# Kernel tuning notes

Hardware: AMD Instinct MI355X
Metric: run time of the kernel (lower is better)

Reference implementation:

```python
import jax, jax.numpy as jnp
import numpy as np

D_IN, D_DICT, K, N = 768, 16384, 32, 8192


def setup_inputs() -> dict:
    key = jax.random.key(0)
    k1, k2, k3, k4, k5 = jax.random.split(key, 5)
    s_in = 1.0 / np.sqrt(D_IN)
    s_dict = 1.0 / np.sqrt(D_DICT)
    return {
        "x": jax.random.normal(k1, (N, D_IN), dtype=jnp.float32),
        # torch Linear: weight [out, in], bias [out]
        "W_enc": jax.random.uniform(k2, (D_DICT, D_IN), jnp.float32, -s_in, s_in),
        "b_enc": jax.random.uniform(k3, (D_DICT,), jnp.float32, -s_in, s_in),
        "W_dec": jax.random.uniform(k4, (D_IN, D_DICT), jnp.float32, -s_dict, s_dict),
        "b_dec": jax.random.uniform(k5, (D_IN,), jnp.float32, -s_dict, s_dict),
    }


def reference(x, W_enc, b_enc, W_dec, b_dec):
    # encode: z = x @ W_enc^T + b_enc  -> [N, d_dict]
    z = jnp.einsum("nd,kd->nk", x, W_enc) + b_enc
    # top-k mask along last dim (scatter 1.0 at top-k indices)
    _, idx = jax.lax.top_k(z, K)                      # idx: [N, K]
    rows = jnp.arange(z.shape[0])[:, None]            # [N, 1]
    mask = jnp.zeros_like(z).at[rows, idx].set(1.0)
    z_sparse = z * mask
    # decode: x_hat = z_sparse @ W_dec^T + b_dec -> [N, d_in]
    x_hat = jnp.einsum("nk,dk->nd", z_sparse, W_dec) + b_dec
    return (x_hat, z_sparse)
```

## Files before the change

### kernel.cpp

```cpp
#include <hip/hip_runtime.h>
#include <stdint.h>

#define D_IN   768
#define D_DICT 16384
#define NROWS  8192
#define TOPK   32
#define CAND_TARGET 40
#define CAND_MAX    80

typedef __attribute__((ext_vector_type(4))) float  f32x4;
typedef __attribute__((ext_vector_type(8))) short  s16x8;
typedef __attribute__((ext_vector_type(4))) unsigned short u16x4;

static __device__ __forceinline__ unsigned short f2bf(float f) {
    unsigned int u = __float_as_uint(f);
    unsigned int r = (u + 0x7FFFu + ((u >> 16) & 1u)) >> 16;
    return (unsigned short)r;
}
static __device__ __forceinline__ unsigned short bfmap(unsigned short u) {
    return (u & 0x8000u) ? (unsigned short)(~u) : (unsigned short)(u | 0x8000u);
}

static __device__ __forceinline__ void gload_lds16(const void* g, void* l) {
    __builtin_amdgcn_global_load_lds(
        (const __attribute__((address_space(1))) unsigned int*)g,
        (__attribute__((address_space(3))) unsigned int*)l, 16, 0, 0);
}

__global__ __launch_bounds__(256) void cast_bf16(const float4* __restrict__ in,
                                                 u16x4* __restrict__ out, int n4) {
    int idx = blockIdx.x * 256 + threadIdx.x;
    if (idx >= n4) return;
    float4 v = in[idx];
    u16x4 o;
    o.x = f2bf(v.x); o.y = f2bf(v.y); o.z = f2bf(v.z); o.w = f2bf(v.w);
    out[idx] = o;
}

__global__ void transpose_wdec(const float* __restrict__ in, float* __restrict__ out) {
    __shared__ float t[32][33];
    int bx = blockIdx.x, by = blockIdx.y;
    int tx = threadIdx.x, ty = threadIdx.y;
#pragma unroll
    for (int i = 0; i < 4; ++i)
        t[ty + i * 8][tx] = in[(size_t)(by * 32 + ty + i * 8) * D_DICT + bx * 32 + tx];
    __syncthreads();
#pragma unroll
    for (int i = 0; i < 4; ++i)
        out[(size_t)(bx * 32 + ty + i * 8) * D_IN + by * 32 + tx] = t[tx][ty + i * 8];
}

__global__ __launch_bounds__(256) void gemm_enc(const unsigned short* __restrict__ Xb,
                                                const unsigned short* __restrict__ Wb,
                                                const float* __restrict__ bEnc,
                                                unsigned short* __restrict__ zhat) {
    __shared__ unsigned short As[128 * 64];
    __shared__ unsigned short Bs[128 * 64];
    const int tid    = threadIdx.x;
    const int waveId = tid >> 6;
    const int lane   = tid & 63;
    const int rowBase = blockIdx.y * 128;
    const int colBase = blockIdx.x * 128;
    const int wm = waveId >> 1, wn = waveId & 1;

    f32x4 acc[4][4] = {};

    const int m0 = wm * 64 + (lane & 15);
    const int n0 = wn * 64 + (lane & 15);
    const int quad = lane >> 4;
    const int xa = m0 & 7;
    const int xb = n0 & 7;

    for (int k0 = 0; k0 < D_IN; k0 += 64) {
#pragma unroll
        for (int i = 0; i < 4; ++i) {
            int slot = i * 256 + tid;
            int r = slot >> 3;
            int cc = ((slot & 7) ^ (r & 7)) * 8;
            const unsigned short* ga = Xb + (size_t)(rowBase + r) * D_IN + k0 + cc;
            const unsigned short* gb = Wb + (size_t)(colBase + r) * D_IN + k0 + cc;
            unsigned short* la = As + (size_t)(i * 256 + waveId * 64) * 8;
            unsigned short* lb = Bs + (size_t)(i * 256 + waveId * 64) * 8;
            gload_lds16(ga, la);
            gload_lds16(gb, lb);
        }
        __syncthreads();
#pragma unroll
        for (int kk = 0; kk < 2; ++kk) {
            const int ch = kk * 4 + quad;
            s16x8 a[4], b[4];
#pragma unroll
            for (int t = 0; t < 4; ++t) {
                a[t] = *(const s16x8*)(As + (m0 + t * 16) * 64 + ((ch ^ xa) << 3));
                b[t] = *(const s16x8*)(Bs + (n0 + t * 16) * 64 + ((ch ^ xb) << 3));
            }
#pragma unroll
            for (int mi = 0; mi < 4; ++mi)
#pragma unroll
                for (int ni = 0; ni < 4; ++ni)
                    acc[mi][ni] = __builtin_amdgcn_mfma_f32_16x16x32_bf16(
                        a[mi], b[ni], acc[mi][ni], 0, 0, 0);
        }
        __syncthreads();
    }

    const int col0 = colBase + wn * 64 + (lane & 15);
    const int rq   = (lane >> 4) * 4;
#pragma unroll
    for (int ni = 0; ni < 4; ++ni) {
        int gc = col0 + ni * 16;
        float bias = bEnc[gc];
#pragma unroll
        for (int mi = 0; mi < 4; ++mi) {
            int gr0 = rowBase + wm * 64 + mi * 16 + rq;
#pragma unroll
            for (int rg = 0; rg < 4; ++rg) {
                float v = acc[mi][ni][rg] + bias;
                zhat[(size_t)(gr0 + rg) * D_DICT + gc] = bfmap(f2bf(v));
            }
        }
    }
}

__global__ __launch_bounds__(256) void sel_dec(const unsigned short* __restrict__ zhat,
                                               const float* __restrict__ x,
                                               const float* __restrict__ wEnc,
                                               const float* __restrict__ bEnc,
                                               const float* __restrict__ wDecT,
                                               const float* __restrict__ bDec,
                                               float* __restrict__ zsp,
                                               float* __restrict__ xhat) {
    const int row = blockIdx.x;
    const int tid = threadIdx.x;
    const int waveId = tid >> 6;

    __shared__ int   histc[4][256];
    __shared__ float xs[D_IN];
    __shared__ int   cidx[CAND_MAX];
    __shared__ float zc[CAND_MAX];
    __shared__ int   selk[TOPK];
    __shared__ float selv[TOPK];
    __shared__ int   sh_bin, sh_cum, sh_bin2;
    __shared__ int   sh_nstrict, sh_ntie, sh_nsel;

    uint4 r[8];
    const uint4* zr4 = (const uint4*)(zhat + (size_t)row * D_DICT);
#pragma unroll
    for (int i = 0; i < 8; ++i) r[i] = zr4[i * 256 + tid];

    {
        float4 z4 = make_float4(0.f, 0.f, 0.f, 0.f);
        float4* zd = (float4*)(zsp + (size_t)row * D_DICT);
#pragma unroll
        for (int i = 0; i < 16; ++i) zd[i * 256 + tid] = z4;
    }

    for (int j = tid; j < D_IN; j += 256) xs[j] = x[(size_t)row * D_IN + j];
    if (tid == 0) { sh_nstrict = 0; sh_ntie = 0; sh_nsel = 0; }

    unsigned int floorU = 0xBF80u;
    int shift1 = 6;
    const int T = CAND_TARGET;

    for (int att = 0; att < 2; ++att) {
        for (int b = tid; b < 1024; b += 256) ((int*)histc)[b] = 0;
        if (tid == 0) sh_bin = -1;
        __syncthreads();
#pragma unroll
        for (int i = 0; i < 8; ++i) {
            unsigned int w[4] = {r[i].x, r[i].y, r[i].z, r[i].w};
#pragma unroll
            for (int q = 0; q < 4; ++q)
#pragma unroll
                for (int h = 0; h < 2; ++h) {
                    unsigned int u = (w[q] >> (16 * h)) & 0xFFFFu;
                    if (u >= floorU) {
                        int bin = (int)((u - floorU) >> shift1);
                        if (bin > 255) bin = 255;
                        atomicAdd(&histc[waveId][bin], 1);
                    }
                }
        }
        __syncthreads();
        if (tid < 256) histc[0][tid] += histc[1][tid] + histc[2][tid] + histc[3][tid];
        __syncthreads();
        if (tid < 64) {
            int l = tid;
            int b0 = 255 - l * 4;
            int s0 = histc[0][b0], s1 = histc[0][b0 - 1],
                s2 = histc[0][b0 - 2], s3 = histc[0][b0 - 3];
            int local = s0 + s1 + s2 + s3;
            int pref = local;
#pragma unroll
            for (int off = 1; off < 64; off <<= 1) {
                int n = __shfl_up(pref, off, 64);
                if (l >= off) pref += n;
            }
            unsigned long long m = __ballot(pref >= T);
            if (m) {
                int first = (int)__ffsll(m) - 1;
                if (l == first) {
                    int cum = pref - local;
                    int b, c;
                    if      (cum + s0 >= T)           { b = b0;     c = cum; }
                    else if (cum + s0 + s1 >= T)      { b = b0 - 1; c = cum + s0; }
                    else if (cum + s0 + s1 + s2 >= T) { b = b0 - 2; c = cum + s0 + s1; }
                    else                              { b = b0 - 3; c = cum + s0 + s1 + s2; }
                    sh_bin = b; sh_cum = c;
                }
            }
        }
        __syncthreads();
        if (sh_bin >= 0) break;
        floorU = 0u; shift1 = 8;
    }
    const int b1 = sh_bin;
    const int cumAbove = sh_cum;
    const int s2 = shift1 - 6;

    for (int b = tid; b < 1024; b += 256) ((int*)histc)[b] = 0;
    __syncthreads();
#pragma unroll
    for (int i = 0; i < 8; ++i) {
        unsigned int w[4] = {r[i].x, r[i].y, r[i].z, r[i].w};
#pragma unroll
        for (int q = 0; q < 4; ++q)
#pragma unroll
            for (int h = 0; h < 2; ++h) {
                unsigned int u = (w[q] >> (16 * h)) & 0xFFFFu;
                if (u >= floorU) {
                    int bin = (int)((u - floorU) >> shift1);
                    if (bin > 255) bin = 255;
                    if (bin == b1) {
                        int bin2 = (int)(((u - floorU) >> s2) & 63u);
                        atomicAdd(&histc[waveId][bin2], 1);
                    }
                }
            }
    }
    __syncthreads();
    if (tid < 64) {
        int l = tid;
        int bb = 63 - l;
        int local = histc[0][bb] + histc[1][bb] + histc[2][bb] + histc[3][bb];
        int pref = local;
#pragma unroll
        for (int off = 1; off < 64; off <<= 1) {
            int n = __shfl_up(pref, off, 64);
            if (l >= off) pref += n;
        }
        unsigned long long m = __ballot(cumAbove + pref >= T);
        int first = (int)__ffsll(m) - 1;
        if (l == first) sh_bin2 = bb;
    }
    __syncthreads();
    const unsigned int tieLo  = floorU + ((unsigned)b1 << shift1) + ((unsigned)sh_bin2 << s2);
    const unsigned int tieTop = tieLo + (1u << s2) - 1u;

#pragma unroll
    for (int i = 0; i < 8; ++i) {
        unsigned int w[4] = {r[i].x, r[i].y, r[i].z, r[i].w};
#pragma unroll
        for (int q = 0; q < 4; ++q)
#pragma unroll
            for (int h = 0; h < 2; ++h) {
                unsigned int u = (w[q] >> (16 * h)) & 0xFFFFu;
                if (u > tieTop) {
                    int p = atomicAdd(&sh_nstrict, 1);
                    cidx[p] = (i * 256 + tid) * 8 + q * 2 + h;
                } else if (u >= tieLo) {
                    int t = atomicAdd(&sh_ntie, 1);
                    if (t < CAND_TARGET) cidx[CAND_MAX - 1 - t] = (i * 256 + tid) * 8 + q * 2 + h;
                }
            }
    }
    __syncthreads();
    const int nstrict = sh_nstrict;
    const int nt = min(sh_ntie, CAND_TARGET);
    int tmpv = 0;
    if (tid < nt) tmpv = cidx[CAND_MAX - 1 - tid];
    __syncthreads();
    if (tid < nt) cidx[nstrict + tid] = tmpv;
    __syncthreads();
    const int nc = nstrict + nt;

    const int sub = tid & 3;
    const int cq  = tid >> 2;
    for (int c0 = 0; c0 < nc; c0 += 64) {
        int c = c0 + cq;
        double acc = 0.0;
        int k = 0;
        if (c < nc) {
            k = cidx[c];
            const float* w  = wEnc + (size_t)k * D_IN + sub * 192;
            const float* xp = xs + sub * 192;
#pragma unroll 8
            for (int j = 0; j < 192; ++j) acc += (double)xp[j] * (double)w[j];
        }
        acc += __shfl_xor(acc, 1, 64);
        acc += __shfl_xor(acc, 2, 64);
        if (c < nc && sub == 0) zc[c] = (float)(acc + (double)bEnc[k]);
    }
    __syncthreads();

    if (tid < nc) {
        float v = zc[tid];
        int   k = cidx[tid];
        int rk = 0;
        for (int j = 0; j < nc; ++j) {
            float vj = zc[j];
            if (vj > v || (vj == v && cidx[j] < k)) ++rk;
        }
        if (rk < TOPK) {
            int s = atomicAdd(&sh_nsel, 1);
            selk[s] = k; selv[s] = v;
        }
    }
    __syncthreads();

    if (tid < TOPK) zsp[(size_t)row * D_DICT + selk[tid]] = selv[tid];

    for (int d = tid; d < D_IN; d += 256) {
        float acc = bDec[d];
#pragma unroll
        for (int j = 0; j < TOPK; ++j)
            acc += selv[j] * wDecT[(size_t)selk[j] * D_IN + d];
        xhat[(size_t)row * D_IN + d] = acc;
    }
}

extern "C" void kernel_launch(void* const* d_in, const int* in_sizes, int n_in,
                              void* d_out, int out_size, void* d_ws, size_t ws_size,
                              hipStream_t stream) {
    const float* x    = (const float*)d_in[0];
    const float* wEnc = (const float*)d_in[1];
    const float* bEnc = (const float*)d_in[2];
    const float* wDec = (const float*)d_in[3];
    const float* bDec = (const float*)d_in[4];

    float* xhat = (float*)d_out;
    float* zsp  = (float*)d_out + (size_t)NROWS * D_IN;

    char* ws = (char*)d_ws;
    unsigned short* Xb   = (unsigned short*)ws;
    unsigned short* Wb   = (unsigned short*)(ws + (size_t)NROWS * D_IN * 2);
    float*          WdT  = (float*)(ws + (size_t)NROWS * D_IN * 2
                                       + (size_t)D_DICT * D_IN * 2);
    unsigned short* zhat = (unsigned short*)(ws + 88080384);

    {
        int n4 = NROWS * D_IN / 4;
        cast_bf16<<<(n4 + 255) / 256, 256, 0, stream>>>((const float4*)x, (u16x4*)Xb, n4);
    }
    {
        int n4 = D_DICT * D_IN / 4;
        cast_bf16<<<(n4 + 255) / 256, 256, 0, stream>>>((const float4*)wEnc, (u16x4*)Wb, n4);
    }
    transpose_wdec<<<dim3(D_DICT / 32, D_IN / 32), dim3(32, 8), 0, stream>>>(wDec, WdT);
    gemm_enc<<<dim3(D_DICT / 128, NROWS / 128), 256, 0, stream>>>(Xb, Wb, bEnc, zhat);
    sel_dec<<<NROWS, 256, 0, stream>>>(zhat, x, wEnc, bEnc, WdT, bDec, zsp, xhat);
}
```

Measured before the change: 1.317 ms.

## Move z_sparse zeroing into encoder GEMM and vectorize selection/decode loads

Zeroing of the dense z_sparse output moves from the select/decode kernel into the encoder GEMM, where each block clears its 128x128 tile before computing. That store traffic can then overlap the MFMA work, and sel_dec gets shorter. The candidate rescoring now uses float4 loads with 8 lanes per candidate and four double accumulators, and the decode loop uses float4 loads over 192 threads. The GEMM takes on extra store traffic, and the double-precision rescoring sums in a different order.

Result: no change. 1.297 ms (-1.5%).

```diff
diff --git a/kernel.cpp b/kernel.cpp
--- a/kernel.cpp
+++ b/kernel.cpp
@@ -53,7 +53,8 @@
 __global__ __launch_bounds__(256) void gemm_enc(const unsigned short* __restrict__ Xb,
                                                 const unsigned short* __restrict__ Wb,
                                                 const float* __restrict__ bEnc,
-                                                unsigned short* __restrict__ zhat) {
+                                                unsigned short* __restrict__ zhat,
+                                                float* __restrict__ zsp) {
     __shared__ unsigned short As[128 * 64];
     __shared__ unsigned short Bs[128 * 64];
     const int tid    = threadIdx.x;
@@ -62,6 +63,18 @@
     const int rowBase = blockIdx.y * 128;
     const int colBase = blockIdx.x * 128;
     const int wm = waveId >> 1, wn = waveId & 1;
+
+    {
+        float4 z4 = make_float4(0.f, 0.f, 0.f, 0.f);
+        float4* zd = (float4*)(zsp + (size_t)rowBase * D_DICT + colBase);
+#pragma unroll
+        for (int i = 0; i < 16; ++i) {
+            int slot = i * 256 + tid;
+            int rr = slot >> 5;
+            int cc = slot & 31;
+            zd[(size_t)rr * (D_DICT / 4) + cc] = z4;
+        }
+    }
 
     f32x4 acc[4][4] = {};
 
@@ -135,7 +148,7 @@
     const int waveId = tid >> 6;
 
     __shared__ int   histc[4][256];
-    __shared__ float xs[D_IN];
+    alignas(16) __shared__ float xs[D_IN];
     __shared__ int   cidx[CAND_MAX];
     __shared__ float zc[CAND_MAX];
     __shared__ int   selk[TOPK];
@@ -148,14 +161,8 @@
 #pragma unroll
     for (int i = 0; i < 8; ++i) r[i] = zr4[i * 256 + tid];
 
-    {
-        float4 z4 = make_float4(0.f, 0.f, 0.f, 0.f);
-        float4* zd = (float4*)(zsp + (size_t)row * D_DICT);
-#pragma unroll
-        for (int i = 0; i < 16; ++i) zd[i * 256 + tid] = z4;
-    }
-
-    for (int j = tid; j < D_IN; j += 256) xs[j] = x[(size_t)row * D_IN + j];
+    if (tid < 192)
+        ((float4*)xs)[tid] = ((const float4*)(x + (size_t)row * D_IN))[tid];
     if (tid == 0) { sh_nstrict = 0; sh_ntie = 0; sh_nsel = 0; }
 
     unsigned int floorU = 0xBF80u;
@@ -284,21 +291,30 @@
     __syncthreads();
     const int nc = nstrict + nt;
 
-    const int sub = tid & 3;
-    const int cq  = tid >> 2;
-    for (int c0 = 0; c0 < nc; c0 += 64) {
+    const int sub = tid & 7;
+    const int cq  = tid >> 3;
+    for (int c0 = 0; c0 < nc; c0 += 32) {
         int c = c0 + cq;
-        double acc = 0.0;
+        double a0 = 0.0, a1 = 0.0, a2 = 0.0, a3 = 0.0;
         int k = 0;
         if (c < nc) {
             k = cidx[c];
-            const float* w  = wEnc + (size_t)k * D_IN + sub * 192;
-            const float* xp = xs + sub * 192;
+            const float4* wp = (const float4*)(wEnc + (size_t)k * D_IN);
+            const float4* xp = (const float4*)xs;
 #pragma unroll 8
-            for (int j = 0; j < 192; ++j) acc += (double)xp[j] * (double)w[j];
-        }
+            for (int j = 0; j < 24; ++j) {
+                float4 wv = wp[j * 8 + sub];
+                float4 xv = xp[j * 8 + sub];
+                a0 += (double)xv.x * (double)wv.x;
+                a1 += (double)xv.y * (double)wv.y;
+                a2 += (double)xv.z * (double)wv.z;
+                a3 += (double)xv.w * (double)wv.w;
+            }
+        }
+        double acc = (a0 + a1) + (a2 + a3);
         acc += __shfl_xor(acc, 1, 64);
         acc += __shfl_xor(acc, 2, 64);
+        acc += __shfl_xor(acc, 4, 64);
         if (c < nc && sub == 0) zc[c] = (float)(acc + (double)bEnc[k]);
     }
     __syncthreads();
@@ -320,12 +336,17 @@
 
     if (tid < TOPK) zsp[(size_t)row * D_DICT + selk[tid]] = selv[tid];
 
-    for (int d = tid; d < D_IN; d += 256) {
-        float acc = bDec[d];
-#pragma unroll
-        for (int j = 0; j < TOPK; ++j)
-            acc += selv[j] * wDecT[(size_t)selk[j] * D_IN + d];
-        xhat[(size_t)row * D_IN + d] = acc;
+    if (tid < 192) {
+        float4 acc = ((const float4*)bDec)[tid];
+#pragma unroll 8
+        for (int j = 0; j < TOPK; ++j) {
+            const float4* wr = (const float4*)(wDecT + (size_t)selk[j] * D_IN);
+            float4 wv = wr[tid];
+            float s = selv[j];
+            acc.x += s * wv.x; acc.y += s * wv.y;
+            acc.z += s * wv.z; acc.w += s * wv.w;
+        }
+        ((float4*)(xhat + (size_t)row * D_IN))[tid] = acc;
     }
 }
 
@@ -357,6 +378,6 @@
         cast_bf16<<<(n4 + 255) / 256, 256, 0, stream>>>((const float4*)wEnc, (u16x4*)Wb, n4);
     }
     transpose_wdec<<<dim3(D_DICT / 32, D_IN / 32), dim3(32, 8), 0, stream>>>(wDec, WdT);
-    gemm_enc<<<dim3(D_DICT / 128, NROWS / 128), 256, 0, stream>>>(Xb, Wb, bEnc, zhat);
+    gemm_enc<<<dim3(D_DICT / 128, NROWS / 128), 256, 0, stream>>>(Xb, Wb, bEnc, zhat, zsp);
     sel_dec<<<NROWS, 256, 0, stream>>>(zhat, x, wEnc, bEnc, WdT, bDec, zsp, xhat);
 }
```
